# Optimization experiments

Measured on AMD Instinct MI355X. Metric: run time of the kernel, lower is better.

Reference implementation:

```python
import jax, jax.numpy as jnp
import numpy as np

N_NODES = 50000
N_EDGES = 800000
IN_DIM = 256
HID = 128
OUT = 128
HEADS = 2
EDGE_DIM = 2
NEG_SLOPE = 0.2


def _add_self_loops(src, dst, edge_attr, n):
    # PyG add_self_loops with fill_value='mean': self-loop edge_attr is the
    # mean of edge_attr over edges entering each node (0 if no in-edges).
    sums = jax.ops.segment_sum(edge_attr, dst, num_segments=n)
    cnt = jax.ops.segment_sum(jnp.ones((edge_attr.shape[0],), edge_attr.dtype), dst, num_segments=n)
    loop_attr = sums / jnp.maximum(cnt, 1.0)[:, None]
    ar = jnp.arange(n, dtype=src.dtype)
    return (jnp.concatenate([src, ar]), jnp.concatenate([dst, ar]),
            jnp.concatenate([edge_attr, loop_attr], axis=0))


def _gat_conv(x, src, dst, edge_attr, W, att_src, att_dst, We, att_e, bias, H, C):
    n = x.shape[0]
    xh = (x @ W).reshape(n, H, C)                      # [N,H,C]
    a_src = jnp.sum(xh * att_src, axis=-1)             # [N,H]
    a_dst = jnp.sum(xh * att_dst, axis=-1)             # [N,H]
    eh = (edge_attr @ We).reshape(-1, H, C)            # [E,H,C]
    a_e = jnp.sum(eh * att_e, axis=-1)                 # [E,H]
    logits = jax.nn.leaky_relu(a_src[src] + a_dst[dst] + a_e, NEG_SLOPE)
    # segment softmax over destination node
    m = jax.ops.segment_max(logits, dst, num_segments=n)
    m = jnp.where(jnp.isfinite(m), m, 0.0)
    ex = jnp.exp(logits - m[dst])
    denom = jax.ops.segment_sum(ex, dst, num_segments=n)
    alpha = ex / (denom[dst] + 1e-16)                  # [E,H]
    msg = xh[src] * alpha[:, :, None]                  # [E,H,C]
    out = jax.ops.segment_sum(msg, dst, num_segments=n)  # [N,H,C]
    return out.reshape(n, H * C) + bias


def setup_inputs() -> dict:
    key = jax.random.key(0)
    ks = jax.random.split(key, 16)
    s = 0.05
    inp = {
        "x": jax.random.normal(ks[0], (N_NODES, IN_DIM), jnp.float32),
        "edge_index": jax.random.randint(ks[1], (2, N_EDGES), 0, N_NODES, jnp.int32),
        "edge_attr": jax.random.normal(ks[2], (N_EDGES, EDGE_DIM), jnp.float32),
        # conv1: heads=2
        "W1": jax.random.normal(ks[3], (IN_DIM, HEADS * HID), jnp.float32) * s,
        "att_src1": jax.random.normal(ks[4], (HEADS, HID), jnp.float32) * s,
        "att_dst1": jax.random.normal(ks[5], (HEADS, HID), jnp.float32) * s,
        "We1": jax.random.normal(ks[6], (EDGE_DIM, HEADS * HID), jnp.float32) * s,
        "att_e1": jax.random.normal(ks[7], (HEADS, HID), jnp.float32) * s,
        "b1": jnp.zeros((HEADS * HID,), jnp.float32),
        # conv2: heads=1
        "W2": jax.random.normal(ks[8], (HEADS * HID, OUT), jnp.float32) * s,
        "att_src2": jax.random.normal(ks[9], (1, OUT), jnp.float32) * s,
        "att_dst2": jax.random.normal(ks[10], (1, OUT), jnp.float32) * s,
        "We2": jax.random.normal(ks[11], (EDGE_DIM, OUT), jnp.float32) * s,
        "att_e2": jax.random.normal(ks[12], (1, OUT), jnp.float32) * s,
        "b2": jnp.zeros((OUT,), jnp.float32),
    }
    return inp


def reference(x, edge_index, edge_attr, W1, att_src1, att_dst1, We1, att_e1, b1,
              W2, att_src2, att_dst2, We2, att_e2, b2):
    src, dst = edge_index[0], edge_index[1]
    src, dst, ea = _add_self_loops(src, dst, edge_attr, x.shape[0])
    h = _gat_conv(x, src, dst, ea, W1, att_src1, att_dst1, We1, att_e1, b1, HEADS, HID)
    h = jax.nn.elu(h)
    out = _gat_conv(h, src, dst, ea, W2, att_src2, att_dst2, We2, att_e2, b2, 1, OUT)
    return out
```

## Files before the change

kernel.cpp:

```cpp
#include <hip/hip_runtime.h>
#include <math.h>

#define N_NODES 50000
#define N_EDGES 800000
#define EP (N_EDGES + N_NODES)
#define NEG_SLOPE 0.2f
#define SCAN_BLOCKS ((N_NODES + 255) / 256)

typedef __attribute__((ext_vector_type(8))) short bf16x8;
typedef __attribute__((ext_vector_type(4))) float f32x4;

__device__ __forceinline__ unsigned short f2bf(float f) {
  unsigned u = __float_as_uint(f);
  unsigned r = (u + 0x7FFFu + ((u >> 16) & 1u)) >> 16;
  return (unsigned short)r;
}
__device__ __forceinline__ float bf2f(unsigned short b) {
  return __uint_as_float(((unsigned)b) << 16);
}

__global__ void fill_u32(unsigned* p, unsigned v, int n) {
  int i = blockIdx.x * blockDim.x + threadIdx.x;
  if (i < n) p[i] = v;
}

__global__ void rank_pass8(const int* __restrict__ ei, int* __restrict__ cnt8,
                           int* __restrict__ rank) {
  int e = blockIdx.x * blockDim.x + threadIdx.x;
  if (e >= N_EDGES) return;
  int c = blockIdx.x & 7;
  rank[e] = atomicAdd(&cnt8[c * N_NODES + ei[N_EDGES + e]], 1);
}

__global__ void combine8(int* __restrict__ cnt8, int* __restrict__ cnt) {
  int n = blockIdx.x * blockDim.x + threadIdx.x;
  if (n >= N_NODES) return;
  int running = 0;
  #pragma unroll
  for (int c = 0; c < 8; ++c) {
    int v = cnt8[c * N_NODES + n];
    cnt8[c * N_NODES + n] = running;
    running += v;
  }
  cnt[n] = running;
}

__global__ void block_sums(const int* __restrict__ cnt, int* __restrict__ bsum) {
  __shared__ int ws[4];
  int b = blockIdx.x;
  int i = b * 256 + threadIdx.x;
  int v = (i < N_NODES) ? (cnt[i] + 1) : 0;
  #pragma unroll
  for (int off = 32; off > 0; off >>= 1) v += __shfl_down(v, off);
  if ((threadIdx.x & 63) == 0) ws[threadIdx.x >> 6] = v;
  __syncthreads();
  if (threadIdx.x == 0) bsum[b] = ws[0] + ws[1] + ws[2] + ws[3];
}

__global__ void emit_rowptr(const int* __restrict__ cnt, const int* __restrict__ bsum,
                            int* __restrict__ rowptr) {
  __shared__ int buf[2][256];
  int b = blockIdx.x, t = threadIdx.x;
  int vb = (t < SCAN_BLOCKS) ? bsum[t] : 0;
  buf[0][t] = vb;
  __syncthreads();
  int cur = 0;
  for (int off = 1; off < 256; off <<= 1) {
    int x = buf[cur][t];
    if (t >= off) x += buf[cur][t - off];
    buf[cur ^ 1][t] = x;
    cur ^= 1;
    __syncthreads();
  }
  int base = buf[cur][b] - ((b < SCAN_BLOCKS) ? bsum[b] : 0);
  __syncthreads();
  int i = b * 256 + t;
  int v = (i < N_NODES) ? (cnt[i] + 1) : 0;
  buf[cur][t] = v;
  __syncthreads();
  int c2 = cur;
  for (int off = 1; off < 256; off <<= 1) {
    int x = buf[c2][t];
    if (t >= off) x += buf[c2][t - off];
    buf[c2 ^ 1][t] = x;
    c2 ^= 1;
    __syncthreads();
  }
  int incl = buf[c2][t];
  if (i < N_NODES) {
    rowptr[i] = base + incl - v;
    if (i == N_NODES - 1) rowptr[N_NODES] = base + incl;
  }
}

__global__ void scatter_pass(const int* __restrict__ ei, const float* __restrict__ ea,
                             const int* __restrict__ rowptr, const int* __restrict__ rank,
                             const int* __restrict__ cnt8, uint2* __restrict__ ecsr) {
  int e = blockIdx.x * blockDim.x + threadIdx.x;
  if (e >= N_EDGES) return;
  int d = ei[N_EDGES + e];
  int c = blockIdx.x & 7;
  int pos = rowptr[d] + cnt8[c * N_NODES + d] + rank[e];
  uint2 v;
  v.x = (unsigned)ei[e];
  v.y = (unsigned)f2bf(ea[2 * e]) | ((unsigned)f2bf(ea[2 * e + 1]) << 16);
  ecsr[pos] = v;
}

#define MISC_LATTR 196
#define MISC_BT    384
__global__ void prep_misc(const int* __restrict__ rowptr, uint2* __restrict__ ecsr,
                          const float* __restrict__ W1, const float* __restrict__ W2,
                          unsigned short* __restrict__ b1h, unsigned short* __restrict__ b1l,
                          unsigned short* __restrict__ b2h, unsigned short* __restrict__ b2l,
                          const float* __restrict__ ae1, const float* __restrict__ ae2,
                          const float* __restrict__ We1, const float* __restrict__ We2,
                          float* __restrict__ Ae) {
  int b = blockIdx.x;
  int t = threadIdx.x;
  if (b < MISC_LATTR) {
    int n = b * 256 + t;
    if (n >= N_NODES) return;
    int beg = rowptr[n], end = rowptr[n + 1];
    float s0 = 0.f, s1 = 0.f;
    for (int j = beg; j < end - 1; ++j) {
      unsigned p = ecsr[j].y;
      s0 += __uint_as_float(p << 16);
      s1 += __uint_as_float(p & 0xFFFF0000u);
    }
    float c = fmaxf((float)(end - 1 - beg), 1.0f);
    uint2 m;
    m.x = (unsigned)n;
    m.y = (unsigned)f2bf(s0 / c) | ((unsigned)f2bf(s1 / c) << 16);
    ecsr[end - 1] = m;
  } else if (b < MISC_LATTR + MISC_BT) {
    int nb = b - MISC_LATTR;
    float v; unsigned short* ph; unsigned short* pl; int idx;
    if (nb < 256) { v = W1[t * 256 + nb];         ph = b1h; pl = b1l; idx = nb * 256 + t; }
    else          { v = W2[t * 128 + (nb - 256)]; ph = b2h; pl = b2l; idx = (nb - 256) * 256 + t; }
    unsigned short h = f2bf(v);
    ph[idx] = h;
    pl[idx] = f2bf(v - bf2f(h));
  } else {
    if (t >= 64) return;
    int bb = b - (MISC_LATTR + MISC_BT);
    float s = 0.f;
    if (bb < 4) {
      int d = bb >> 1, h = bb & 1;
      for (int c = t; c < 128; c += 64)
        s += We1[d * 256 + h * 128 + c] * ae1[h * 128 + c];
    } else {
      int d = bb - 4;
      for (int c = t; c < 128; c += 64)
        s += We2[d * 128 + c] * ae2[c];
    }
    for (int off = 32; off > 0; off >>= 1) s += __shfl_down(s, off);
    if (t == 0) Ae[bb] = s;
  }
}

template <int H>
__global__ __launch_bounds__(256) void gemm_split(
    const float* __restrict__ A,
    const unsigned short* __restrict__ Bth, const unsigned short* __restrict__ Btl,
    unsigned short* __restrict__ C, int M, int N,
    const float* __restrict__ att_src, const float* __restrict__ att_dst,
    float* __restrict__ asrc, float* __restrict__ adst) {
  __shared__ __attribute__((aligned(16))) unsigned short As[2][64][40];
  __shared__ __attribute__((aligned(16))) unsigned short Bs[2][128][40];
  __shared__ float redS[2][64], redD[2][64];
  int bm = blockIdx.y * 64, bn = blockIdx.x * 128;
  int tid = threadIdx.x;
  int l = tid & 63;
  int wid = tid >> 6;
  int wr = wid >> 1, wc = wid & 1;
  int rr = l & 15, kc = l >> 4;

  f32x4 acc[2][4];
  #pragma unroll
  for (int i = 0; i < 2; ++i)
    #pragma unroll
    for (int j = 0; j < 4; ++j)
      acc[i][j] = (f32x4){0.f, 0.f, 0.f, 0.f};

  int ar = tid >> 2, ac = tid & 3;
  int gm = bm + ar;

  for (int kt = 0; kt < 8; ++kt) {
    int k0 = kt * 32;
    float4 f0 = {0.f, 0.f, 0.f, 0.f}, f1 = f0;
    if (gm < M) {
      f0 = *(const float4*)(A + (size_t)gm * 256 + k0 + ac * 8);
      f1 = *(const float4*)(A + (size_t)gm * 256 + k0 + ac * 8 + 4);
    }
    float f[8] = {f0.x, f0.y, f0.z, f0.w, f1.x, f1.y, f1.z, f1.w};
    unsigned hw[4], lw[4];
    #pragma unroll
    for (int q = 0; q < 4; ++q) {
      unsigned short ha = f2bf(f[2 * q]),  hb = f2bf(f[2 * q + 1]);
      unsigned short la = f2bf(f[2 * q] - bf2f(ha)), lb = f2bf(f[2 * q + 1] - bf2f(hb));
      hw[q] = (unsigned)ha | ((unsigned)hb << 16);
      lw[q] = (unsigned)la | ((unsigned)lb << 16);
    }
    *(uint4*)&As[0][ar][ac * 8] = make_uint4(hw[0], hw[1], hw[2], hw[3]);
    *(uint4*)&As[1][ar][ac * 8] = make_uint4(lw[0], lw[1], lw[2], lw[3]);
    #pragma unroll
    for (int p = 0; p < 2; ++p) {
      int id = tid + p * 256;
      int nn = id >> 2, cc = id & 3;
      *(uint4*)&Bs[0][nn][cc * 8] = *(const uint4*)(Bth + (size_t)(bn + nn) * 256 + k0 + cc * 8);
      *(uint4*)&Bs[1][nn][cc * 8] = *(const uint4*)(Btl + (size_t)(bn + nn) * 256 + k0 + cc * 8);
    }
    __syncthreads();
    bf16x8 ah[2], alo[2], bh[4], bl[4];
    #pragma unroll
    for (int i = 0; i < 2; ++i) {
      ah[i]  = *(const bf16x8*)&As[0][wr * 32 + i * 16 + rr][kc * 8];
      alo[i] = *(const bf16x8*)&As[1][wr * 32 + i * 16 + rr][kc * 8];
    }
    #pragma unroll
    for (int j = 0; j < 4; ++j) {
      bh[j] = *(const bf16x8*)&Bs[0][wc * 64 + j * 16 + rr][kc * 8];
      bl[j] = *(const bf16x8*)&Bs[1][wc * 64 + j * 16 + rr][kc * 8];
    }
    #pragma unroll
    for (int i = 0; i < 2; ++i)
      #pragma unroll
      for (int j = 0; j < 4; ++j) {
        acc[i][j] = __builtin_amdgcn_mfma_f32_16x16x32_bf16(ah[i],  bh[j], acc[i][j], 0, 0, 0);
        acc[i][j] = __builtin_amdgcn_mfma_f32_16x16x32_bf16(ah[i],  bl[j], acc[i][j], 0, 0, 0);
        acc[i][j] = __builtin_amdgcn_mfma_f32_16x16x32_bf16(alo[i], bh[j], acc[i][j], 0, 0, 0);
      }
    __syncthreads();
  }

  #pragma unroll
  for (int i = 0; i < 2; ++i)
    #pragma unroll
    for (int reg = 0; reg < 4; ++reg) {
      int row = bm + wr * 32 + i * 16 + kc * 4 + reg;
      if (row < M) {
        #pragma unroll
        for (int j = 0; j < 4; ++j) {
          int col = bn + wc * 64 + j * 16 + rr;
          C[(size_t)row * N + col] = f2bf(acc[i][j][reg]);
        }
      }
    }

  int head = (H == 2) ? (bn >> 7) : 0;
  float ats[4], atd[4];
  #pragma unroll
  for (int j = 0; j < 4; ++j) {
    int colh = wc * 64 + j * 16 + rr;
    ats[j] = att_src[head * 128 + colh];
    atd[j] = att_dst[head * 128 + colh];
  }
  #pragma unroll
  for (int i = 0; i < 2; ++i)
    #pragma unroll
    for (int reg = 0; reg < 4; ++reg) {
      float sp = acc[i][0][reg] * ats[0] + acc[i][1][reg] * ats[1] +
                 acc[i][2][reg] * ats[2] + acc[i][3][reg] * ats[3];
      float dp = acc[i][0][reg] * atd[0] + acc[i][1][reg] * atd[1] +
                 acc[i][2][reg] * atd[2] + acc[i][3][reg] * atd[3];
      #pragma unroll
      for (int off = 1; off < 16; off <<= 1) {
        sp += __shfl_xor(sp, off);
        dp += __shfl_xor(dp, off);
      }
      if (rr == 0) {
        int row_local = wr * 32 + i * 16 + kc * 4 + reg;
        redS[wc][row_local] = sp;
        redD[wc][row_local] = dp;
      }
    }
  __syncthreads();
  if (tid < 64) {
    int row = bm + tid;
    if (row < M) {
      asrc[row * H + head] = redS[0][tid] + redS[1][tid];
      adst[row * H + head] = redD[0][tid] + redD[1][tid];
    }
  }
}

template <int H, int ACT>
__global__ __launch_bounds__(64)
void aggregate_fused(const unsigned short* __restrict__ xh, const float* __restrict__ asrc,
                     const float* __restrict__ adst, const uint2* __restrict__ ecsr,
                     const int* __restrict__ rowptr,
                     const float* __restrict__ Ae, int aeoff,
                     const float* __restrict__ bias, float* __restrict__ out) {
  constexpr int D = H * 128;
  constexpr int COLS = D / 64;
  __shared__ float exl[256][H];
  __shared__ int sl[256];
  int n = blockIdx.x;
  int t = threadIdx.x;
  int beg = rowptr[n], end = rowptr[n + 1];
  int hA = t & (H - 1);
  float adnA = adst[n * H + hA];
  float Ae0 = Ae[aeoff + hA], Ae1 = Ae[aeoff + H + hA];
  int hB = (H == 2) ? (t >> 5) : 0;
  float lsum = 0.f;
  float acc[4][COLS];
  #pragma unroll
  for (int q = 0; q < 4; ++q)
    #pragma unroll
    for (int c = 0; c < COLS; ++c) acc[q][c] = 0.f;

  for (int cbeg = beg; cbeg < end; cbeg += 256) {
    int cnt = min(256, end - cbeg);
    for (int idx = t; idx < cnt * H; idx += 64) {
      int j0 = (H == 2) ? (idx >> 1) : idx;
      uint2 ev = ecsr[cbeg + j0];
      int s = (int)ev.x;
      float ea0 = __uint_as_float(ev.y << 16);
      float ea1 = __uint_as_float(ev.y & 0xFFFF0000u);
      float lg = asrc[s * H + hA] + adnA + ea0 * Ae0 + ea1 * Ae1;
      lg = (lg > 0.f) ? lg : NEG_SLOPE * lg;
      float ex = __expf(lg);
      exl[j0][hA] = ex;
      if (hA == 0) sl[j0] = s;
      lsum += ex;
    }
    __syncthreads();
    int j = 0;
    for (; j + 8 <= cnt; j += 8) {
      #pragma unroll
      for (int q = 0; q < 8; ++q) {
        float e = exl[j + q][hB];
        int s = sl[j + q];
        if (COLS == 4) {
          uint2 u = *(const uint2*)(xh + (size_t)s * D + 4 * t);
          acc[q & 3][0] = fmaf(e, __uint_as_float(u.x << 16), acc[q & 3][0]);
          acc[q & 3][1] = fmaf(e, __uint_as_float(u.x & 0xFFFF0000u), acc[q & 3][1]);
          acc[q & 3][2] = fmaf(e, __uint_as_float(u.y << 16), acc[q & 3][2]);
          acc[q & 3][3] = fmaf(e, __uint_as_float(u.y & 0xFFFF0000u), acc[q & 3][3]);
        } else {
          unsigned u = *(const unsigned*)(xh + (size_t)s * D + 2 * t);
          acc[q & 3][0] = fmaf(e, __uint_as_float(u << 16), acc[q & 3][0]);
          acc[q & 3][1] = fmaf(e, __uint_as_float(u & 0xFFFF0000u), acc[q & 3][1]);
        }
      }
    }
    for (; j < cnt; ++j) {
      float e = exl[j][hB];
      int s = sl[j];
      if (COLS == 4) {
        uint2 u = *(const uint2*)(xh + (size_t)s * D + 4 * t);
        acc[0][0] = fmaf(e, __uint_as_float(u.x << 16), acc[0][0]);
        acc[0][1] = fmaf(e, __uint_as_float(u.x & 0xFFFF0000u), acc[0][1]);
        acc[0][2] = fmaf(e, __uint_as_float(u.y << 16), acc[0][2]);
        acc[0][3] = fmaf(e, __uint_as_float(u.y & 0xFFFF0000u), acc[0][3]);
      } else {
        unsigned u = *(const unsigned*)(xh + (size_t)s * D + 2 * t);
        acc[0][0] = fmaf(e, __uint_as_float(u << 16), acc[0][0]);
        acc[0][1] = fmaf(e, __uint_as_float(u & 0xFFFF0000u), acc[0][1]);
      }
    }
    __syncthreads();
  }

  #pragma unroll
  for (int off = H; off < 64; off <<= 1) lsum += __shfl_xor(lsum, off);
  float tot = (H == 2) ? __shfl(lsum, hB) : lsum;
  float inv = 1.0f / (tot + 1e-16f);

  float v[COLS];
  #pragma unroll
  for (int c = 0; c < COLS; ++c) {
    v[c] = fmaf(inv, (acc[0][c] + acc[1][c]) + (acc[2][c] + acc[3][c]),
                bias[COLS * t + c]);
    if (ACT) v[c] = (v[c] > 0.f) ? v[c] : expm1f(v[c]);
  }
  if (COLS == 4) {
    *(float4*)(out + (size_t)n * D + 4 * t) = make_float4(v[0], v[1], v[2], v[3]);
  } else {
    *(float2*)(out + (size_t)n * D + 2 * t) = make_float2(v[0], v[1]);
  }
}

extern "C" void kernel_launch(void* const* d_in, const int* in_sizes, int n_in,
                              void* d_out, int out_size, void* d_ws, size_t ws_size,
                              hipStream_t stream) {
  const float* x    = (const float*)d_in[0];
  const int*   ei   = (const int*)d_in[1];
  const float* ea   = (const float*)d_in[2];
  const float* W1   = (const float*)d_in[3];
  const float* as1  = (const float*)d_in[4];
  const float* ad1  = (const float*)d_in[5];
  const float* We1  = (const float*)d_in[6];
  const float* ae1  = (const float*)d_in[7];
  const float* b1   = (const float*)d_in[8];
  const float* W2   = (const float*)d_in[9];
  const float* as2  = (const float*)d_in[10];
  const float* ad2  = (const float*)d_in[11];
  const float* We2  = (const float*)d_in[12];
  const float* ae2  = (const float*)d_in[13];
  const float* b2   = (const float*)d_in[14];
  float* out = (float*)d_out;

  char* w = (char*)d_ws;
  size_t off = 0;
  auto alloc = [&](size_t bytes) -> void* {
    void* p = w + off;
    off = (off + bytes + 255) & ~(size_t)255;
    return p;
  };
  unsigned short* xhb   = (unsigned short*)alloc((size_t)N_NODES * 256 * 2);
  float*          hbuf  = (float*)alloc((size_t)N_NODES * 256 * 4);
  unsigned short* B1hi  = (unsigned short*)alloc(256 * 256 * 2);
  unsigned short* B1lo  = (unsigned short*)alloc(256 * 256 * 2);
  unsigned short* B2hi  = (unsigned short*)alloc(128 * 256 * 2);
  unsigned short* B2lo  = (unsigned short*)alloc(128 * 256 * 2);
  int*      rowptr   = (int*)alloc((N_NODES + 1) * 4);
  int*      cnt      = (int*)alloc(N_NODES * 4);
  int*      cnt8     = (int*)alloc((size_t)N_NODES * 8 * 4);
  int*      rank     = (int*)alloc((size_t)N_EDGES * 4);
  int*      bsum     = (int*)alloc(256 * 4);
  uint2*    ecsr     = (uint2*)alloc((size_t)EP * 8);
  float*    asrc     = (float*)alloc(N_NODES * 2 * 4);
  float*    adst     = (float*)alloc(N_NODES * 2 * 4);
  float*    Ae       = (float*)alloc(16 * 4);

  auto cdiv = [](int a, int b) { return (a + b - 1) / b; };

  fill_u32<<<cdiv(N_NODES * 8, 256), 256, 0, stream>>>((unsigned*)cnt8, 0u, N_NODES * 8);
  rank_pass8<<<cdiv(N_EDGES, 256), 256, 0, stream>>>(ei, cnt8, rank);
  combine8<<<cdiv(N_NODES, 256), 256, 0, stream>>>(cnt8, cnt);
  block_sums<<<SCAN_BLOCKS, 256, 0, stream>>>(cnt, bsum);
  emit_rowptr<<<SCAN_BLOCKS, 256, 0, stream>>>(cnt, bsum, rowptr);
  scatter_pass<<<cdiv(N_EDGES, 256), 256, 0, stream>>>(ei, ea, rowptr, rank, cnt8, ecsr);
  prep_misc<<<MISC_LATTR + MISC_BT + 6, 256, 0, stream>>>(rowptr, ecsr, W1, W2,
                                                          B1hi, B1lo, B2hi, B2lo,
                                                          ae1, ae2, We1, We2, Ae);

  gemm_split<2><<<dim3(2, cdiv(N_NODES, 64)), 256, 0, stream>>>(x, B1hi, B1lo, xhb, N_NODES, 256,
                                                                as1, ad1, asrc, adst);
  aggregate_fused<2, 1><<<N_NODES, 64, 0, stream>>>(xhb, asrc, adst, ecsr, rowptr,
                                                    Ae, 0, b1, hbuf);

  gemm_split<1><<<dim3(1, cdiv(N_NODES, 64)), 256, 0, stream>>>(hbuf, B2hi, B2lo, xhb, N_NODES, 128,
                                                                as2, ad2, asrc, adst);
  aggregate_fused<1, 0><<<N_NODES, 64, 0, stream>>>(xhb, asrc, adst, ecsr, rowptr,
                                                    Ae, 4, b2, out);
}
```

Before: 237.2 us.

## Fuse rank pass into GEMM1 launch and compute self-loop terms inside aggregation

```diff
diff --git a/kernel.cpp b/kernel.cpp
--- a/kernel.cpp
+++ b/kernel.cpp
@@ -6,6 +6,9 @@
 #define EP (N_EDGES + N_NODES)
 #define NEG_SLOPE 0.2f
 #define SCAN_BLOCKS ((N_NODES + 255) / 256)
+#define GEMM1B (2 * ((N_NODES + 63) / 64))
+#define RANKB ((N_EDGES + 255) / 256)
+#define FILLB ((N_NODES * 8 + 255) / 256)
 
 typedef __attribute__((ext_vector_type(8))) short bf16x8;
 typedef __attribute__((ext_vector_type(4))) float f32x4;
@@ -19,42 +22,201 @@
   return __uint_as_float(((unsigned)b) << 16);
 }
 
-__global__ void fill_u32(unsigned* p, unsigned v, int n) {
-  int i = blockIdx.x * blockDim.x + threadIdx.x;
-  if (i < n) p[i] = v;
-}
-
-__global__ void rank_pass8(const int* __restrict__ ei, int* __restrict__ cnt8,
-                           int* __restrict__ rank) {
-  int e = blockIdx.x * blockDim.x + threadIdx.x;
-  if (e >= N_EDGES) return;
-  int c = blockIdx.x & 7;
-  rank[e] = atomicAdd(&cnt8[c * N_NODES + ei[N_EDGES + e]], 1);
-}
-
-__global__ void combine8(int* __restrict__ cnt8, int* __restrict__ cnt) {
-  int n = blockIdx.x * blockDim.x + threadIdx.x;
-  if (n >= N_NODES) return;
+__global__ void prep_inputs(int* __restrict__ cnt8,
+                            const float* __restrict__ W1, const float* __restrict__ W2,
+                            unsigned short* __restrict__ b1h, unsigned short* __restrict__ b1l,
+                            unsigned short* __restrict__ b2h, unsigned short* __restrict__ b2l,
+                            const float* __restrict__ ae1, const float* __restrict__ ae2,
+                            const float* __restrict__ We1, const float* __restrict__ We2,
+                            float* __restrict__ Ae) {
+  int b = blockIdx.x;
+  int t = threadIdx.x;
+  if (b < FILLB) {
+    int i = b * 256 + t;
+    if (i < N_NODES * 8) cnt8[i] = 0;
+  } else if (b < FILLB + 384) {
+    int nb = b - FILLB;
+    float v; unsigned short* ph; unsigned short* pl; int idx;
+    if (nb < 256) { v = W1[t * 256 + nb];         ph = b1h; pl = b1l; idx = nb * 256 + t; }
+    else          { v = W2[t * 128 + (nb - 256)]; ph = b2h; pl = b2l; idx = (nb - 256) * 256 + t; }
+    unsigned short h = f2bf(v);
+    ph[idx] = h;
+    pl[idx] = f2bf(v - bf2f(h));
+  } else {
+    if (t >= 64) return;
+    int bb = b - (FILLB + 384);
+    float s = 0.f;
+    if (bb < 4) {
+      int d = bb >> 1, h = bb & 1;
+      for (int c = t; c < 128; c += 64)
+        s += We1[d * 256 + h * 128 + c] * ae1[h * 128 + c];
+    } else {
+      int d = bb - 4;
+      for (int c = t; c < 128; c += 64)
+        s += We2[d * 128 + c] * ae2[c];
+    }
+    for (int off = 32; off > 0; off >>= 1) s += __shfl_down(s, off);
+    if (t == 0) Ae[bb] = s;
+  }
+}
+
+__global__ __launch_bounds__(256) void gemm1_rank(
+    const float* __restrict__ A,
+    const unsigned short* __restrict__ Bth, const unsigned short* __restrict__ Btl,
+    unsigned short* __restrict__ C,
+    const float* __restrict__ att_src, const float* __restrict__ att_dst,
+    float* __restrict__ asrc, float* __restrict__ adst,
+    const int* __restrict__ ei, int* __restrict__ cnt8, int* __restrict__ rank) {
+  __shared__ __attribute__((aligned(16))) unsigned short As[2][64][40];
+  __shared__ __attribute__((aligned(16))) unsigned short Bs[2][128][40];
+  __shared__ float redS[2][64], redD[2][64];
+  int tid = threadIdx.x;
+
+  if (blockIdx.x >= GEMM1B) {
+    int bl = blockIdx.x - GEMM1B;
+    int e = bl * 256 + tid;
+    if (e < N_EDGES)
+      rank[e] = atomicAdd(&cnt8[(bl & 7) * N_NODES + ei[N_EDGES + e]], 1);
+    return;
+  }
+
+  const int M = N_NODES, N = 256;
+  int bm = (blockIdx.x >> 1) * 64, bn = (blockIdx.x & 1) * 128;
+  int l = tid & 63;
+  int wid = tid >> 6;
+  int wr = wid >> 1, wc = wid & 1;
+  int rr = l & 15, kc = l >> 4;
+
+  f32x4 acc[2][4];
+  #pragma unroll
+  for (int i = 0; i < 2; ++i)
+    #pragma unroll
+    for (int j = 0; j < 4; ++j)
+      acc[i][j] = (f32x4){0.f, 0.f, 0.f, 0.f};
+
+  int ar = tid >> 2, ac = tid & 3;
+  int gm = bm + ar;
+
+  for (int kt = 0; kt < 8; ++kt) {
+    int k0 = kt * 32;
+    float4 f0 = {0.f, 0.f, 0.f, 0.f}, f1 = f0;
+    if (gm < M) {
+      f0 = *(const float4*)(A + (size_t)gm * 256 + k0 + ac * 8);
+      f1 = *(const float4*)(A + (size_t)gm * 256 + k0 + ac * 8 + 4);
+    }
+    float f[8] = {f0.x, f0.y, f0.z, f0.w, f1.x, f1.y, f1.z, f1.w};
+    unsigned hw[4], lw[4];
+    #pragma unroll
+    for (int q = 0; q < 4; ++q) {
+      unsigned short ha = f2bf(f[2 * q]),  hb = f2bf(f[2 * q + 1]);
+      unsigned short la = f2bf(f[2 * q] - bf2f(ha)), lb = f2bf(f[2 * q + 1] - bf2f(hb));
+      hw[q] = (unsigned)ha | ((unsigned)hb << 16);
+      lw[q] = (unsigned)la | ((unsigned)lb << 16);
+    }
+    *(uint4*)&As[0][ar][ac * 8] = make_uint4(hw[0], hw[1], hw[2], hw[3]);
+    *(uint4*)&As[1][ar][ac * 8] = make_uint4(lw[0], lw[1], lw[2], lw[3]);
+    #pragma unroll
+    for (int p = 0; p < 2; ++p) {
+      int id = tid + p * 256;
+      int nn = id >> 2, cc = id & 3;
+      *(uint4*)&Bs[0][nn][cc * 8] = *(const uint4*)(Bth + (size_t)(bn + nn) * 256 + k0 + cc * 8);
+      *(uint4*)&Bs[1][nn][cc * 8] = *(const uint4*)(Btl + (size_t)(bn + nn) * 256 + k0 + cc * 8);
+    }
+    __syncthreads();
+    bf16x8 ah[2], alo[2], bh[4], bl[4];
+    #pragma unroll
+    for (int i = 0; i < 2; ++i) {
+      ah[i]  = *(const bf16x8*)&As[0][wr * 32 + i * 16 + rr][kc * 8];
+      alo[i] = *(const bf16x8*)&As[1][wr * 32 + i * 16 + rr][kc * 8];
+    }
+    #pragma unroll
+    for (int j = 0; j < 4; ++j) {
+      bh[j] = *(const bf16x8*)&Bs[0][wc * 64 + j * 16 + rr][kc * 8];
+      bl[j] = *(const bf16x8*)&Bs[1][wc * 64 + j * 16 + rr][kc * 8];
+    }
+    #pragma unroll
+    for (int i = 0; i < 2; ++i)
+      #pragma unroll
+      for (int j = 0; j < 4; ++j) {
+        acc[i][j] = __builtin_amdgcn_mfma_f32_16x16x32_bf16(ah[i],  bh[j], acc[i][j], 0, 0, 0);
+        acc[i][j] = __builtin_amdgcn_mfma_f32_16x16x32_bf16(ah[i],  bl[j], acc[i][j], 0, 0, 0);
+        acc[i][j] = __builtin_amdgcn_mfma_f32_16x16x32_bf16(alo[i], bh[j], acc[i][j], 0, 0, 0);
+      }
+    __syncthreads();
+  }
+
+  #pragma unroll
+  for (int i = 0; i < 2; ++i)
+    #pragma unroll
+    for (int reg = 0; reg < 4; ++reg) {
+      int row = bm + wr * 32 + i * 16 + kc * 4 + reg;
+      if (row < M) {
+        #pragma unroll
+        for (int j = 0; j < 4; ++j) {
+          int col = bn + wc * 64 + j * 16 + rr;
+          C[(size_t)row * N + col] = f2bf(acc[i][j][reg]);
+        }
+      }
+    }
+
+  int head = bn >> 7;
+  float ats[4], atd[4];
+  #pragma unroll
+  for (int j = 0; j < 4; ++j) {
+    int colh = wc * 64 + j * 16 + rr;
+    ats[j] = att_src[head * 128 + colh];
+    atd[j] = att_dst[head * 128 + colh];
+  }
+  #pragma unroll
+  for (int i = 0; i < 2; ++i)
+    #pragma unroll
+    for (int reg = 0; reg < 4; ++reg) {
+      float sp = acc[i][0][reg] * ats[0] + acc[i][1][reg] * ats[1] +
+                 acc[i][2][reg] * ats[2] + acc[i][3][reg] * ats[3];
+      float dp = acc[i][0][reg] * atd[0] + acc[i][1][reg] * atd[1] +
+                 acc[i][2][reg] * atd[2] + acc[i][3][reg] * atd[3];
+      #pragma unroll
+      for (int off = 1; off < 16; off <<= 1) {
+        sp += __shfl_xor(sp, off);
+        dp += __shfl_xor(dp, off);
+      }
+      if (rr == 0) {
+        int row_local = wr * 32 + i * 16 + kc * 4 + reg;
+        redS[wc][row_local] = sp;
+        redD[wc][row_local] = dp;
+      }
+    }
+  __syncthreads();
+  if (tid < 64) {
+    int row = bm + tid;
+    if (row < M) {
+      asrc[row * 2 + head] = redS[0][tid] + redS[1][tid];
+      adst[row * 2 + head] = redD[0][tid] + redD[1][tid];
+    }
+  }
+}
+
+__global__ void combine_bsum(int* __restrict__ cnt8, int* __restrict__ cnt,
+                             int* __restrict__ bsum) {
+  __shared__ int ws[4];
+  int b = blockIdx.x, t = threadIdx.x;
+  int n = b * 256 + t;
   int running = 0;
-  #pragma unroll
-  for (int c = 0; c < 8; ++c) {
-    int v = cnt8[c * N_NODES + n];
-    cnt8[c * N_NODES + n] = running;
-    running += v;
-  }
-  cnt[n] = running;
-}
-
-__global__ void block_sums(const int* __restrict__ cnt, int* __restrict__ bsum) {
-  __shared__ int ws[4];
-  int b = blockIdx.x;
-  int i = b * 256 + threadIdx.x;
-  int v = (i < N_NODES) ? (cnt[i] + 1) : 0;
+  if (n < N_NODES) {
+    #pragma unroll
+    for (int c = 0; c < 8; ++c) {
+      int v = cnt8[c * N_NODES + n];
+      cnt8[c * N_NODES + n] = running;
+      running += v;
+    }
+    cnt[n] = running;
+  }
+  int v = (n < N_NODES) ? (running + 1) : 0;
   #pragma unroll
   for (int off = 32; off > 0; off >>= 1) v += __shfl_down(v, off);
-  if ((threadIdx.x & 63) == 0) ws[threadIdx.x >> 6] = v;
+  if ((t & 63) == 0) ws[t >> 6] = v;
   __syncthreads();
-  if (threadIdx.x == 0) bsum[b] = ws[0] + ws[1] + ws[2] + ws[3];
+  if (t == 0) bsum[b] = ws[0] + ws[1] + ws[2] + ws[3];
 }
 
 __global__ void emit_rowptr(const int* __restrict__ cnt, const int* __restrict__ bsum,
@@ -107,60 +269,7 @@
   ecsr[pos] = v;
 }
 
-#define MISC_LATTR 196
-#define MISC_BT    384
-__global__ void prep_misc(const int* __restrict__ rowptr, uint2* __restrict__ ecsr,
-                          const float* __restrict__ W1, const float* __restrict__ W2,
-                          unsigned short* __restrict__ b1h, unsigned short* __restrict__ b1l,
-                          unsigned short* __restrict__ b2h, unsigned short* __restrict__ b2l,
-                          const float* __restrict__ ae1, const float* __restrict__ ae2,
-                          const float* __restrict__ We1, const float* __restrict__ We2,
-                          float* __restrict__ Ae) {
-  int b = blockIdx.x;
-  int t = threadIdx.x;
-  if (b < MISC_LATTR) {
-    int n = b * 256 + t;
-    if (n >= N_NODES) return;
-    int beg = rowptr[n], end = rowptr[n + 1];
-    float s0 = 0.f, s1 = 0.f;
-    for (int j = beg; j < end - 1; ++j) {
-      unsigned p = ecsr[j].y;
-      s0 += __uint_as_float(p << 16);
-      s1 += __uint_as_float(p & 0xFFFF0000u);
-    }
-    float c = fmaxf((float)(end - 1 - beg), 1.0f);
-    uint2 m;
-    m.x = (unsigned)n;
-    m.y = (unsigned)f2bf(s0 / c) | ((unsigned)f2bf(s1 / c) << 16);
-    ecsr[end - 1] = m;
-  } else if (b < MISC_LATTR + MISC_BT) {
-    int nb = b - MISC_LATTR;
-    float v; unsigned short* ph; unsigned short* pl; int idx;
-    if (nb < 256) { v = W1[t * 256 + nb];         ph = b1h; pl = b1l; idx = nb * 256 + t; }
-    else          { v = W2[t * 128 + (nb - 256)]; ph = b2h; pl = b2l; idx = (nb - 256) * 256 + t; }
-    unsigned short h = f2bf(v);
-    ph[idx] = h;
-    pl[idx] = f2bf(v - bf2f(h));
-  } else {
-    if (t >= 64) return;
-    int bb = b - (MISC_LATTR + MISC_BT);
-    float s = 0.f;
-    if (bb < 4) {
-      int d = bb >> 1, h = bb & 1;
-      for (int c = t; c < 128; c += 64)
-        s += We1[d * 256 + h * 128 + c] * ae1[h * 128 + c];
-    } else {
-      int d = bb - 4;
-      for (int c = t; c < 128; c += 64)
-        s += We2[d * 128 + c] * ae2[c];
-    }
-    for (int off = 32; off > 0; off >>= 1) s += __shfl_down(s, off);
-    if (t == 0) Ae[bb] = s;
-  }
-}
-
-template <int H>
-__global__ __launch_bounds__(256) void gemm_split(
+__global__ __launch_bounds__(256) void gemm_split1(
     const float* __restrict__ A,
     const unsigned short* __restrict__ Bth, const unsigned short* __restrict__ Btl,
     unsigned short* __restrict__ C, int M, int N,
@@ -248,13 +357,12 @@
       }
     }
 
-  int head = (H == 2) ? (bn >> 7) : 0;
   float ats[4], atd[4];
   #pragma unroll
   for (int j = 0; j < 4; ++j) {
     int colh = wc * 64 + j * 16 + rr;
-    ats[j] = att_src[head * 128 + colh];
-    atd[j] = att_dst[head * 128 + colh];
+    ats[j] = att_src[colh];
+    atd[j] = att_dst[colh];
   }
   #pragma unroll
   for (int i = 0; i < 2; ++i)
@@ -279,8 +387,8 @@
   if (tid < 64) {
     int row = bm + tid;
     if (row < M) {
-      asrc[row * H + head] = redS[0][tid] + redS[1][tid];
-      adst[row * H + head] = redD[0][tid] + redD[1][tid];
+      asrc[row] = redS[0][tid] + redS[1][tid];
+      adst[row] = redD[0][tid] + redD[1][tid];
     }
   }
 }
@@ -298,20 +406,21 @@
   __shared__ int sl[256];
   int n = blockIdx.x;
   int t = threadIdx.x;
-  int beg = rowptr[n], end = rowptr[n + 1];
+  int beg = rowptr[n], endE = rowptr[n + 1] - 1;
   int hA = t & (H - 1);
   float adnA = adst[n * H + hA];
   float Ae0 = Ae[aeoff + hA], Ae1 = Ae[aeoff + H + hA];
   int hB = (H == 2) ? (t >> 5) : 0;
   float lsum = 0.f;
+  float sea0 = 0.f, sea1 = 0.f;
   float acc[4][COLS];
   #pragma unroll
   for (int q = 0; q < 4; ++q)
     #pragma unroll
     for (int c = 0; c < COLS; ++c) acc[q][c] = 0.f;
 
-  for (int cbeg = beg; cbeg < end; cbeg += 256) {
-    int cnt = min(256, end - cbeg);
+  for (int cbeg = beg; cbeg < endE; cbeg += 256) {
+    int cnt = min(256, endE - cbeg);
     for (int idx = t; idx < cnt * H; idx += 64) {
       int j0 = (H == 2) ? (idx >> 1) : idx;
       uint2 ev = ecsr[cbeg + j0];
@@ -322,7 +431,7 @@
       lg = (lg > 0.f) ? lg : NEG_SLOPE * lg;
       float ex = __expf(lg);
       exl[j0][hA] = ex;
-      if (hA == 0) sl[j0] = s;
+      if (hA == 0) { sl[j0] = s; sea0 += ea0; sea1 += ea1; }
       lsum += ex;
     }
     __syncthreads();
@@ -364,9 +473,48 @@
   }
 
   #pragma unroll
+  for (int off = 1; off < 64; off <<= 1) {
+    sea0 += __shfl_xor(sea0, off);
+    sea1 += __shfl_xor(sea1, off);
+  }
+  float cdeg = fmaxf((float)(endE - beg), 1.0f);
+  float m0 = sea0 / cdeg, m1 = sea1 / cdeg;
+
+  float eL[2];
+  if (H == 2) {
+    float2 av = *(const float2*)(asrc + 2 * n);
+    float2 dv = *(const float2*)(adst + 2 * n);
+    #pragma unroll
+    for (int h = 0; h < 2; ++h) {
+      float lg = ((h == 0) ? av.x : av.y) + ((h == 0) ? dv.x : dv.y) +
+                 m0 * Ae[aeoff + h] + m1 * Ae[aeoff + 2 + h];
+      lg = (lg > 0.f) ? lg : NEG_SLOPE * lg;
+      eL[h] = __expf(lg);
+    }
+  } else {
+    float lg = asrc[n] + adst[n] + m0 * Ae[aeoff] + m1 * Ae[aeoff + 1];
+    lg = (lg > 0.f) ? lg : NEG_SLOPE * lg;
+    eL[0] = __expf(lg);
+    eL[1] = 0.f;
+  }
+
+  #pragma unroll
   for (int off = H; off < 64; off <<= 1) lsum += __shfl_xor(lsum, off);
   float tot = (H == 2) ? __shfl(lsum, hB) : lsum;
-  float inv = 1.0f / (tot + 1e-16f);
+  float eSelf = (H == 2) ? eL[hB] : eL[0];
+  float inv = 1.0f / (tot + eSelf + 1e-16f);
+
+  if (COLS == 4) {
+    uint2 u = *(const uint2*)(xh + (size_t)n * D + 4 * t);
+    acc[0][0] = fmaf(eSelf, __uint_as_float(u.x << 16), acc[0][0]);
+    acc[0][1] = fmaf(eSelf, __uint_as_float(u.x & 0xFFFF0000u), acc[0][1]);
+    acc[0][2] = fmaf(eSelf, __uint_as_float(u.y << 16), acc[0][2]);
+    acc[0][3] = fmaf(eSelf, __uint_as_float(u.y & 0xFFFF0000u), acc[0][3]);
+  } else {
+    unsigned u = *(const unsigned*)(xh + (size_t)n * D + 2 * t);
+    acc[0][0] = fmaf(eSelf, __uint_as_float(u << 16), acc[0][0]);
+    acc[0][1] = fmaf(eSelf, __uint_as_float(u & 0xFFFF0000u), acc[0][1]);
+  }
 
   float v[COLS];
   #pragma unroll
@@ -427,23 +575,18 @@
 
   auto cdiv = [](int a, int b) { return (a + b - 1) / b; };
 
-  fill_u32<<<cdiv(N_NODES * 8, 256), 256, 0, stream>>>((unsigned*)cnt8, 0u, N_NODES * 8);
-  rank_pass8<<<cdiv(N_EDGES, 256), 256, 0, stream>>>(ei, cnt8, rank);
-  combine8<<<cdiv(N_NODES, 256), 256, 0, stream>>>(cnt8, cnt);
-  block_sums<<<SCAN_BLOCKS, 256, 0, stream>>>(cnt, bsum);
+  prep_inputs<<<FILLB + 384 + 6, 256, 0, stream>>>(cnt8, W1, W2, B1hi, B1lo, B2hi, B2lo,
+                                                   ae1, ae2, We1, We2, Ae);
+  gemm1_rank<<<GEMM1B + RANKB, 256, 0, stream>>>(x, B1hi, B1lo, xhb, as1, ad1, asrc, adst,
+                                                 ei, cnt8, rank);
+  combine_bsum<<<SCAN_BLOCKS, 256, 0, stream>>>(cnt8, cnt, bsum);
   emit_rowptr<<<SCAN_BLOCKS, 256, 0, stream>>>(cnt, bsum, rowptr);
-  scatter_pass<<<cdiv(N_EDGES, 256), 256, 0, stream>>>(ei, ea, rowptr, rank, cnt8, ecsr);
-  prep_misc<<<MISC_LATTR + MISC_BT + 6, 256, 0, stream>>>(rowptr, ecsr, W1, W2,
-                                                          B1hi, B1lo, B2hi, B2lo,
-                                                          ae1, ae2, We1, We2, Ae);
-
-  gemm_split<2><<<dim3(2, cdiv(N_NODES, 64)), 256, 0, stream>>>(x, B1hi, B1lo, xhb, N_NODES, 256,
-                                                                as1, ad1, asrc, adst);
+  scatter_pass<<<RANKB, 256, 0, stream>>>(ei, ea, rowptr, rank, cnt8, ecsr);
+
   aggregate_fused<2, 1><<<N_NODES, 64, 0, stream>>>(xhb, asrc, adst, ecsr, rowptr,
                                                     Ae, 0, b1, hbuf);
-
-  gemm_split<1><<<dim3(1, cdiv(N_NODES, 64)), 256, 0, stream>>>(hbuf, B2hi, B2lo, xhb, N_NODES, 128,
-                                                                as2, ad2, asrc, adst);
+  gemm_split1<<<dim3(1, cdiv(N_NODES, 64)), 256, 0, stream>>>(hbuf, B2hi, B2lo, xhb, N_NODES, 128,
+                                                              as2, ad2, asrc, adst);
   aggregate_fused<1, 0><<<N_NODES, 64, 0, stream>>>(xhb, asrc, adst, ecsr, rowptr,
                                                     Ae, 4, b2, out);
 }
```

Measured after the change: 214.7 us. -9.4%, faster.
